# Optimization experiments

Measured on AMD Instinct MI355X. Metric: run time of the kernel, lower is better.

## Reference

```python
import jax, jax.numpy as jnp
import numpy as np

D_MODEL, D_K, D_V, N_HEADS = 1024, 64, 64, 16
B, S = 8, 1024
NEG = -1e9
LN_EPS = 1e-5


def setup_inputs() -> dict:
    key = jax.random.key(0)
    ks = jax.random.split(key, 10)
    scale = 1.0 / np.sqrt(D_MODEL)
    return {
        "Q_in": jax.random.normal(ks[0], (B, S, D_MODEL), jnp.float32),
        "K_in": jax.random.normal(ks[1], (B, S, D_MODEL), jnp.float32),
        "V_in": jax.random.normal(ks[2], (B, S, D_MODEL), jnp.float32),
        "mask": jax.random.randint(ks[3], (B, S, S), 0, 2).astype(bool),
        "W_Q": jax.random.normal(ks[4], (D_MODEL, N_HEADS * D_K), jnp.float32) * scale,
        "W_K": jax.random.normal(ks[5], (D_MODEL, N_HEADS * D_K), jnp.float32) * scale,
        "W_V": jax.random.normal(ks[6], (D_MODEL, N_HEADS * D_V), jnp.float32) * scale,
        "W_fc": jax.random.normal(ks[7], (N_HEADS * D_V, D_MODEL), jnp.float32) * scale,
        "ln_gamma": jnp.ones((D_MODEL,), jnp.float32),
        "ln_beta": jnp.zeros((D_MODEL,), jnp.float32),
    }


def reference(Q_in, K_in, V_in, mask, W_Q, W_K, W_V, W_fc, ln_gamma, ln_beta):
    b = Q_in.shape[0]
    # projections -> (B, H, S, d)
    Q = (Q_in @ W_Q).reshape(b, -1, N_HEADS, D_K).transpose(0, 2, 1, 3)
    K = (K_in @ W_K).reshape(b, -1, N_HEADS, D_K).transpose(0, 2, 1, 3)
    V = (V_in @ W_V).reshape(b, -1, N_HEADS, D_V).transpose(0, 2, 1, 3)
    # scores (B, H, Sq, Sk)
    scores = jnp.einsum("bhqd,bhkd->bhqk", Q, K) / np.sqrt(D_K)
    scores = jnp.where(mask[:, None, :, :], NEG, scores)
    attn = jax.nn.softmax(scores, axis=-1)
    context = jnp.einsum("bhqk,bhkd->bhqd", attn, V)
    context = context.transpose(0, 2, 1, 3).reshape(b, -1, N_HEADS * D_V)
    out = context @ W_fc + Q_in  # residual
    mu = jnp.mean(out, axis=-1, keepdims=True)
    var = jnp.var(out, axis=-1, keepdims=True)
    out = (out - mu) * jax.lax.rsqrt(var + LN_EPS) * ln_gamma + ln_beta
    return out, attn
```

## Files before the change

kernel.cpp:

```cpp
#include <hip/hip_runtime.h>
#include <stdint.h>

typedef unsigned short u16;
typedef float f32x4 __attribute__((ext_vector_type(4)));
typedef short s16x8 __attribute__((ext_vector_type(8)));
typedef short s16x4 __attribute__((ext_vector_type(4)));
typedef int   i32x4 __attribute__((ext_vector_type(4)));

constexpr int B  = 8;
constexpr int S  = 1024;
constexpr int DM = 1024;
constexpr int H  = 16;
constexpr int M  = B * S;
constexpr float NEGINF = -1e9f;

__device__ __forceinline__ u16 f2bf(float f) {
    union { float f; uint32_t u; } v; v.f = f;
    uint32_t u = v.u;
    uint32_t r = 0x7FFFu + ((u >> 16) & 1u);
    return (u16)((u + r) >> 16);
}
__device__ __forceinline__ float bf2f(u16 h) {
    union { uint32_t u; float f; } v; v.u = ((uint32_t)h) << 16; return v.f;
}

__device__ __forceinline__ void gload16(const u16* g, u16* l) {
    __builtin_amdgcn_global_load_lds(
        (const __attribute__((address_space(1))) unsigned int*)g,
        (__attribute__((address_space(3))) unsigned int*)l, 16, 0, 0);
}

__global__ void cvt_all(const float* __restrict__ q, const float* __restrict__ k,
                        const float* __restrict__ v,
                        u16* __restrict__ xq, u16* __restrict__ xk, u16* __restrict__ xv) {
    const float* in; u16* out;
    if (blockIdx.y == 0)      { in = q; out = xq; }
    else if (blockIdx.y == 1) { in = k; out = xk; }
    else                      { in = v; out = xv; }
    int i = (blockIdx.x * 256 + threadIdx.x) * 4;
    float4 val = *(const float4*)(in + i);
    ushort4 o;
    o.x = f2bf(val.x); o.y = f2bf(val.y); o.z = f2bf(val.z); o.w = f2bf(val.w);
    *(ushort4*)(out + i) = o;
}

__global__ void transpose_all(const float* __restrict__ w0, const float* __restrict__ w1,
                              const float* __restrict__ w2, const float* __restrict__ w3,
                              u16* __restrict__ o0, u16* __restrict__ o1,
                              u16* __restrict__ o2, u16* __restrict__ o3) {
    const float* W; u16* Wt;
    switch (blockIdx.z) {
        case 0:  W = w0; Wt = o0; break;
        case 1:  W = w1; Wt = o1; break;
        case 2:  W = w2; Wt = o2; break;
        default: W = w3; Wt = o3; break;
    }
    __shared__ float tile[32][33];
    int n0 = blockIdx.x * 32, k0 = blockIdx.y * 32;
    int tx = threadIdx.x & 31, ty = threadIdx.x >> 5;
#pragma unroll
    for (int r = 0; r < 4; ++r)
        tile[ty + r*8][tx] = W[(size_t)(k0 + ty + r*8) * DM + n0 + tx];
    __syncthreads();
#pragma unroll
    for (int r = 0; r < 4; ++r)
        Wt[(size_t)(n0 + ty + r*8) * DM + k0 + tx] = f2bf(tile[tx][ty + r*8]);
}

template<int EPI>
__global__ __launch_bounds__(256, 2)
void gemm_bt(const u16* __restrict__ A, const u16* __restrict__ Bt,
             void* __restrict__ Cv, const float* __restrict__ resid)
{
    __shared__ u16 As[128 * 32];
    __shared__ u16 Bs[128 * 32];
    const int m0 = blockIdx.x * 128;
    const int n0 = blockIdx.y * 128;
    const int t = threadIdx.x;
    const int lane = t & 63;
    const int wid = t >> 6;
    const int wm = (wid >> 1) * 64;
    const int wn = (wid & 1) * 64;
    const int lr = lane & 15;
    const int lg = lane >> 4;

    const u16* Ag = A  + (size_t)(m0 + (t >> 2)) * 1024 + (t & 3) * 8;
    const u16* Bg = Bt + (size_t)(n0 + (t >> 2)) * 1024 + (t & 3) * 8;
    u16* Al = As + t * 8;
    u16* Bl = Bs + t * 8;

    f32x4 acc[4][4] = {};

    for (int kt = 0; kt < 32; ++kt) {
        const int ko = kt * 32;
        __syncthreads();
        gload16(Ag + ko,            Al);
        gload16(Ag + 64*1024 + ko,  Al + 64*32);
        gload16(Bg + ko,            Bl);
        gload16(Bg + 64*1024 + ko,  Bl + 64*32);
        __syncthreads();
        s16x8 af[4], bfr[4];
#pragma unroll
        for (int m = 0; m < 4; ++m)
            af[m] = *(const s16x8*)(As + (wm + m*16 + lr) * 32 + lg * 8);
#pragma unroll
        for (int n = 0; n < 4; ++n)
            bfr[n] = *(const s16x8*)(Bs + (wn + n*16 + lr) * 32 + lg * 8);
#pragma unroll
        for (int m = 0; m < 4; ++m)
#pragma unroll
            for (int n = 0; n < 4; ++n)
                acc[m][n] = __builtin_amdgcn_mfma_f32_16x16x32_bf16(af[m], bfr[n], acc[m][n], 0, 0, 0);
    }

#pragma unroll
    for (int m = 0; m < 4; ++m) {
#pragma unroll
        for (int n = 0; n < 4; ++n) {
            const int rg0 = m0 + wm + m*16 + lg*4;
            const int cg  = n0 + wn + n*16 + lr;
            if constexpr (EPI == 0) {
                u16* C = (u16*)Cv;
#pragma unroll
                for (int r = 0; r < 4; ++r)
                    C[(size_t)(rg0 + r) * 1024 + cg] = f2bf(acc[m][n][r]);
            } else if constexpr (EPI == 1) {
                u16* C = (u16*)Cv;
                const int bb = rg0 >> 10;
                const int s0 = rg0 & 1023;
                const int hh = cg >> 6;
                const int dd = cg & 63;
                ushort4 pk;
                pk.x = f2bf(acc[m][n][0]); pk.y = f2bf(acc[m][n][1]);
                pk.z = f2bf(acc[m][n][2]); pk.w = f2bf(acc[m][n][3]);
                *(ushort4*)(C + (size_t)((bb*16 + hh)*64 + dd) * 1024 + s0) = pk;
            } else {
                float* C = (float*)Cv;
#pragma unroll
                for (int r = 0; r < 4; ++r) {
                    size_t idx = (size_t)(rg0 + r) * 1024 + cg;
                    C[idx] = acc[m][n][r] + resid[idx];
                }
            }
        }
    }
}

__global__ __launch_bounds__(256, 2)
void attn_fused(const u16* __restrict__ Qp, const u16* __restrict__ Kp,
                const void* __restrict__ maskp, const u16* __restrict__ Vt,
                float* __restrict__ attn, u16* __restrict__ ctx)
{
    const int i  = blockIdx.x;
    const int qt = (i >> 3) & 63;
    const int g  = ((i >> 9) << 3) | (i & 7);
    const int h  = g & 15;
    const int b  = g >> 4;
    const int q0 = qt * 16;

    const int t = threadIdx.x;
    const int lane = t & 63;
    const int w = t >> 6;
    const int lr = lane & 15;
    const int lg = lane >> 4;

    constexpr int PLD = 1032;
    __shared__ u16 Plds[16][PLD];
    __shared__ float redB[4][16];

    uint32_t orv = 0;
    const uint32_t* mw = (const uint32_t*)maskp;
#pragma unroll
    for (int ii = 0; ii < 64; ++ii) orv |= mw[ii];
    const bool mask_bytes = (orv > 1u);

    const u16* qb = Qp + (size_t)(b*S + q0 + lr) * DM + h*64 + lg*8;
    s16x8 qf0 = *(const s16x8*)(qb);
    s16x8 qf1 = *(const s16x8*)(qb + 32);

    const size_t mrow = (size_t)b * S * S + (size_t)(q0 + lr) * S;

    i32x4 kf0s[2][4], kf1s[2][4], mis[2][4];
    int   mbs[2][4];
    s16x4 paf[16];
    float hs = 0.f;

#define QK_ISSUE(st, nb_) do {                                                      \
    _Pragma("unroll")                                                               \
    for (int j = 0; j < 4; ++j) {                                                   \
        const u16* kb_ = Kp + (size_t)(b*S + w*256 + (nb_)*64 + j*16 + lr) * DM     \
                            + h*64 + lg*8;                                          \
        asm volatile("global_load_dwordx4 %0, %2, off\n\t"                          \
                     "global_load_dwordx4 %1, %2, off offset:64"                    \
                     : "=v"(kf0s[st][j]), "=v"(kf1s[st][j]) : "v"(kb_));            \
        const size_t off_ = mrow + w*256 + (nb_)*64 + j*16 + lg*4;                  \
        if (mask_bytes) {                                                           \
            asm volatile("global_load_dword %0, %1, off"                            \
                         : "=v"(mbs[st][j]) : "v"((const uint8_t*)maskp + off_));   \
        } else {                                                                    \
            asm volatile("global_load_dwordx4 %0, %1, off"                          \
                         : "=v"(mis[st][j]) : "v"((const int*)maskp + off_));       \
        }                                                                           \
    }                                                                               \
} while (0)

#define QK_COMPUTE(st, nb_) do {                                                    \
    _Pragma("unroll")                                                               \
    for (int j = 0; j < 4; ++j) {                                                   \
        const int nk_ = (nb_)*4 + j;                                                \
        s16x8 kf0 = *(const s16x8*)&kf0s[st][j];                                    \
        s16x8 kf1 = *(const s16x8*)&kf1s[st][j];                                    \
        int m0_, m1_, m2_, m3_;                                                     \
        if (mask_bytes) {                                                           \
            int mm = mbs[st][j];                                                    \
            m0_ = mm & 255; m1_ = (mm >> 8) & 255;                                  \
            m2_ = (mm >> 16) & 255; m3_ = ((unsigned)mm) >> 24;                     \
        } else {                                                                    \
            m0_ = mis[st][j][0]; m1_ = mis[st][j][1];                               \
            m2_ = mis[st][j][2]; m3_ = mis[st][j][3];                               \
        }                                                                           \
        f32x4 cc = {};                                                              \
        cc = __builtin_amdgcn_mfma_f32_16x16x32_bf16(kf0, qf0, cc, 0, 0, 0);        \
        cc = __builtin_amdgcn_mfma_f32_16x16x32_bf16(kf1, qf1, cc, 0, 0, 0);        \
        cc[0] = __expf(m0_ ? NEGINF : cc[0] * 0.125f);                              \
        cc[1] = __expf(m1_ ? NEGINF : cc[1] * 0.125f);                              \
        cc[2] = __expf(m2_ ? NEGINF : cc[2] * 0.125f);                              \
        cc[3] = __expf(m3_ ? NEGINF : cc[3] * 0.125f);                              \
        hs += cc[0] + cc[1] + cc[2] + cc[3];                                        \
        s16x4 pa;                                                                   \
        pa[0] = (short)f2bf(cc[0]); pa[1] = (short)f2bf(cc[1]);                     \
        pa[2] = (short)f2bf(cc[2]); pa[3] = (short)f2bf(cc[3]);                     \
        paf[nk_] = pa;                                                              \
        *(s16x4*)&Plds[lr][w*256 + nk_*16 + lg*4] = pa;                             \
    }                                                                               \
} while (0)

    QK_ISSUE(0, 0);
    QK_ISSUE(1, 1);
    asm volatile("s_waitcnt vmcnt(12)");
    __builtin_amdgcn_sched_barrier(0);
    QK_COMPUTE(0, 0);
    QK_ISSUE(0, 2);
    asm volatile("s_waitcnt vmcnt(12)");
    __builtin_amdgcn_sched_barrier(0);
    QK_COMPUTE(1, 1);
    QK_ISSUE(1, 3);
    asm volatile("s_waitcnt vmcnt(12)");
    __builtin_amdgcn_sched_barrier(0);
    QK_COMPUTE(0, 2);
    asm volatile("s_waitcnt vmcnt(0)");
    __builtin_amdgcn_sched_barrier(0);
    QK_COMPUTE(1, 3);
#undef QK_ISSUE
#undef QK_COMPUTE

    hs += __shfl_xor(hs, 16, 64);
    hs += __shfl_xor(hs, 32, 64);
    if (lane < 16) redB[w][lr] = hs;
    __syncthreads();

    const float tot = redB[0][lr] + redB[1][lr] + redB[2][lr] + redB[3][lr];
    const float inv  = tot > 0.f ? 1.0f / tot : 0.f;
    const float fill = tot > 0.f ? 0.f : (1.0f / 1024.0f);
    float invr[4];
#pragma unroll
    for (int r = 0; r < 4; ++r) {
        const int row = lg*4 + r;
        const float tr = redB[0][row] + redB[1][row] + redB[2][row] + redB[3][row];
        invr[r] = tr > 0.f ? 1.0f / tr : 0.f;
    }

    float* arow = attn + (size_t)(b*H + h) * S * S + (size_t)(q0 + lr) * S + w*256 + lg*4;
#pragma unroll
    for (int nk = 0; nk < 16; ++nk) {
        float4 st;
        st.x = fmaf(bf2f((u16)paf[nk][0]), inv, fill);
        st.y = fmaf(bf2f((u16)paf[nk][1]), inv, fill);
        st.z = fmaf(bf2f((u16)paf[nk][2]), inv, fill);
        st.w = fmaf(bf2f((u16)paf[nk][3]), inv, fill);
        *(float4*)(arow + nk*16) = st;
    }

    const u16* vrow = Vt + ((size_t)g*64 + w*16 + lr) * S;
    i32x4 vfs[2][8];
    f32x4 pacc = {};

#define PV_ISSUE(st, kb_) do {                                                      \
    _Pragma("unroll")                                                               \
    for (int j = 0; j < 8; ++j) {                                                   \
        asm volatile("global_load_dwordx4 %0, %1, off"                              \
                     : "=v"(vfs[st][j]) : "v"(vrow + (kb_)*256 + j*32 + lg*8));     \
    }                                                                               \
} while (0)

#define PV_COMPUTE(st, kb_) do {                                                    \
    _Pragma("unroll")                                                               \
    for (int j = 0; j < 8; ++j) {                                                   \
        s16x8 af = *(const s16x8*)&Plds[lr][((kb_)*8 + j)*32 + lg*8];               \
        s16x8 vf = *(const s16x8*)&vfs[st][j];                                      \
        pacc = __builtin_amdgcn_mfma_f32_16x16x32_bf16(af, vf, pacc, 0, 0, 0);      \
    }                                                                               \
} while (0)

    PV_ISSUE(0, 0);
    PV_ISSUE(1, 1);
    asm volatile("s_waitcnt vmcnt(8)");
    __builtin_amdgcn_sched_barrier(0);
    PV_COMPUTE(0, 0);
    PV_ISSUE(0, 2);
    asm volatile("s_waitcnt vmcnt(8)");
    __builtin_amdgcn_sched_barrier(0);
    PV_COMPUTE(1, 1);
    PV_ISSUE(1, 3);
    asm volatile("s_waitcnt vmcnt(8)");
    __builtin_amdgcn_sched_barrier(0);
    PV_COMPUTE(0, 2);
    asm volatile("s_waitcnt vmcnt(0)");
    __builtin_amdgcn_sched_barrier(0);
    PV_COMPUTE(1, 3);
#undef PV_ISSUE
#undef PV_COMPUTE

#pragma unroll
    for (int r = 0; r < 4; ++r)
        ctx[(size_t)(b*S + q0 + lg*4 + r) * DM + h*64 + w*16 + lr] = f2bf(pacc[r] * invr[r]);
}

__global__ __launch_bounds__(256)
void layernorm(const float* __restrict__ x, const float* __restrict__ gamma,
               const float* __restrict__ beta, float* __restrict__ out)
{
    const int row = blockIdx.x;
    const int t = threadIdx.x;
    const float* xr = x + (size_t)row * DM;
    float4 v = *(const float4*)(xr + t*4);
    float s  = v.x + v.y + v.z + v.w;
    float s2 = v.x*v.x + v.y*v.y + v.z*v.z + v.w*v.w;
#pragma unroll
    for (int d = 1; d < 64; d <<= 1) {
        s  += __shfl_xor(s,  d, 64);
        s2 += __shfl_xor(s2, d, 64);
    }
    __shared__ float ls[4], ls2[4];
    if ((t & 63) == 0) { ls[t >> 6] = s; ls2[t >> 6] = s2; }
    __syncthreads();
    s  = ls[0] + ls[1] + ls[2] + ls[3];
    s2 = ls2[0] + ls2[1] + ls2[2] + ls2[3];
    const float mu  = s * (1.0f / DM);
    const float var = s2 * (1.0f / DM) - mu * mu;
    const float rs  = rsqrtf(var + 1e-5f);
    float4 g  = *(const float4*)(gamma + t*4);
    float4 bb = *(const float4*)(beta  + t*4);
    float4 o;
    o.x = (v.x - mu) * rs * g.x + bb.x;
    o.y = (v.y - mu) * rs * g.y + bb.y;
    o.z = (v.z - mu) * rs * g.z + bb.z;
    o.w = (v.w - mu) * rs * g.w + bb.w;
    *(float4*)(out + (size_t)row * DM + t*4) = o;
}

extern "C" void kernel_launch(void* const* d_in, const int* in_sizes, int n_in,
                              void* d_out, int out_size, void* d_ws, size_t ws_size,
                              hipStream_t stream) {
    const float* Qin  = (const float*)d_in[0];
    const float* Kin  = (const float*)d_in[1];
    const float* Vin  = (const float*)d_in[2];
    const void*  mask = d_in[3];
    const float* Wq   = (const float*)d_in[4];
    const float* Wk   = (const float*)d_in[5];
    const float* Wv   = (const float*)d_in[6];
    const float* Wfc  = (const float*)d_in[7];
    const float* gam  = (const float*)d_in[8];
    const float* bet  = (const float*)d_in[9];

    float* out  = (float*)d_out;
    float* attn = (float*)d_out + (size_t)M * DM;

    char* ws = (char*)d_ws;
    constexpr size_t SZ_X = (size_t)M * DM * 2;
    constexpr size_t SZ_W = (size_t)DM * DM * 2;
    u16* Xq  = (u16*)(ws);
    u16* Xk  = (u16*)(ws + SZ_X);
    u16* Xv  = (u16*)(ws + 2*SZ_X);
    u16* WqT = (u16*)(ws + 3*SZ_X);
    u16* WkT = (u16*)(ws + 3*SZ_X + SZ_W);
    u16* WvT = (u16*)(ws + 3*SZ_X + 2*SZ_W);
    u16* WfT = (u16*)(ws + 3*SZ_X + 3*SZ_W);
    u16* Qp  = (u16*)(ws + 3*SZ_X + 4*SZ_W);
    u16* Kp  = (u16*)(ws + 4*SZ_X + 4*SZ_W);
    u16* Vt  = (u16*)(ws + 5*SZ_X + 4*SZ_W);
    float* preLN = (float*)(ws);
    u16*   Ctx   = (u16*)(ws + 2*SZ_X);

    dim3 blk(256);
    cvt_all<<<dim3(M * DM / 1024, 3), blk, 0, stream>>>(Qin, Kin, Vin, Xq, Xk, Xv);
    transpose_all<<<dim3(32, 32, 4), blk, 0, stream>>>(Wq, Wk, Wv, Wfc, WqT, WkT, WvT, WfT);

    gemm_bt<0><<<dim3(64, 8), blk, 0, stream>>>(Xq, WqT, Qp, nullptr);
    gemm_bt<0><<<dim3(64, 8), blk, 0, stream>>>(Xk, WkT, Kp, nullptr);
    gemm_bt<1><<<dim3(64, 8), blk, 0, stream>>>(Xv, WvT, Vt, nullptr);

    attn_fused<<<dim3(8192), blk, 0, stream>>>(Qp, Kp, mask, Vt, attn, Ctx);

    gemm_bt<2><<<dim3(64, 8), blk, 0, stream>>>(Ctx, WfT, preLN, Qin);
    layernorm<<<dim3(M), blk, 0, stream>>>(preLN, gam, bet, out);
}
```

Baseline: 548.0 us.

## Split fused attention into score kernel and separate tiled P·V GEMM

Breaks the fused attention kernel into two. The first computes and stores the normalized attention probabilities. The second is a 128x64-tiled GEMM that re-reads the fp32 attention matrix from global memory, converts it to bf16, and multiplies it by V using double-buffered LDS staging. The aim is to drop the large LDS P buffer, improve occupancy, and get V reuse across 128 query rows instead of 16. The cost is re-reading the full 512MB fp32 attention matrix, which adds a large amount of memory traffic.

```diff
diff --git a/kernel.cpp b/kernel.cpp
--- a/kernel.cpp
+++ b/kernel.cpp
@@ -147,9 +147,8 @@
 }
 
 __global__ __launch_bounds__(256, 2)
-void attn_fused(const u16* __restrict__ Qp, const u16* __restrict__ Kp,
-                const void* __restrict__ maskp, const u16* __restrict__ Vt,
-                float* __restrict__ attn, u16* __restrict__ ctx)
+void attn_scores(const u16* __restrict__ Qp, const u16* __restrict__ Kp,
+                 const void* __restrict__ maskp, float* __restrict__ attn)
 {
     const int i  = blockIdx.x;
     const int qt = (i >> 3) & 63;
@@ -164,8 +163,6 @@
     const int lr = lane & 15;
     const int lg = lane >> 4;
 
-    constexpr int PLD = 1032;
-    __shared__ u16 Plds[16][PLD];
     __shared__ float redB[4][16];
 
     uint32_t orv = 0;
@@ -231,7 +228,6 @@
         pa[0] = (short)f2bf(cc[0]); pa[1] = (short)f2bf(cc[1]);                     \
         pa[2] = (short)f2bf(cc[2]); pa[3] = (short)f2bf(cc[3]);                     \
         paf[nk_] = pa;                                                              \
-        *(s16x4*)&Plds[lr][w*256 + nk_*16 + lg*4] = pa;                             \
     }                                                                               \
 } while (0)
 
@@ -258,17 +254,9 @@
     hs += __shfl_xor(hs, 32, 64);
     if (lane < 16) redB[w][lr] = hs;
     __syncthreads();
-
     const float tot = redB[0][lr] + redB[1][lr] + redB[2][lr] + redB[3][lr];
     const float inv  = tot > 0.f ? 1.0f / tot : 0.f;
     const float fill = tot > 0.f ? 0.f : (1.0f / 1024.0f);
-    float invr[4];
-#pragma unroll
-    for (int r = 0; r < 4; ++r) {
-        const int row = lg*4 + r;
-        const float tr = redB[0][row] + redB[1][row] + redB[2][row] + redB[3][row];
-        invr[r] = tr > 0.f ? 1.0f / tr : 0.f;
-    }
 
     float* arow = attn + (size_t)(b*H + h) * S * S + (size_t)(q0 + lr) * S + w*256 + lg*4;
 #pragma unroll
@@ -280,50 +268,98 @@
         st.w = fmaf(bf2f((u16)paf[nk][3]), inv, fill);
         *(float4*)(arow + nk*16) = st;
     }
-
-    const u16* vrow = Vt + ((size_t)g*64 + w*16 + lr) * S;
-    i32x4 vfs[2][8];
-    f32x4 pacc = {};
-
-#define PV_ISSUE(st, kb_) do {                                                      \
+}
+
+__global__ __launch_bounds__(256, 2)
+void attn_pv_gemm(const float* __restrict__ attn, const u16* __restrict__ Vt,
+                  u16* __restrict__ ctx)
+{
+    __shared__ float Abuf[2][128 * 64];
+    __shared__ u16   Vbuf[2][64 * 64];
+    const int i  = blockIdx.x;
+    const int qt = (i >> 3) & 7;
+    const int g  = ((i >> 6) << 3) | (i & 7);
+    const int h  = g & 15;
+    const int b  = g >> 4;
+    const int q0 = qt * 128;
+
+    const int t = threadIdx.x;
+    const int lane = t & 63;
+    const int w = t >> 6;
+    const int lr = lane & 15;
+    const int lg = lane >> 4;
+
+    const float* abase = attn + (size_t)(b*H + h) * S * S + (size_t)q0 * S;
+    const u16*   vbase = Vt + (size_t)g * 64 * S;
+
+#define PSTAGE(bi, kk) do {                                                         \
+    const int k0_ = (kk) * 64;                                                      \
     _Pragma("unroll")                                                               \
     for (int j = 0; j < 8; ++j) {                                                   \
-        asm volatile("global_load_dwordx4 %0, %1, off"                              \
-                     : "=v"(vfs[st][j]) : "v"(vrow + (kb_)*256 + j*32 + lg*8));     \
+        const int s_ = j*256 + t;                         \
+        const int r_ = s_ >> 4;                                    \
+        const int p_ = s_ & 15;                           \
+        const int l_ = p_ ^ ((r_ & 7) << 1);      \
+        gload16((const u16*)(abase + (size_t)r_ * S + k0_ + l_*4),                  \
+                (u16*)&Abuf[bi][s_ * 4]);                                           \
+    }                                                                               \
+    _Pragma("unroll")                                                               \
+    for (int j = 0; j < 2; ++j) {                                                   \
+        const int s_ = j*256 + t;                                      \
+        const int r_ = s_ >> 3;                                          \
+        const int p_ = s_ & 7;                                                      \
+        const int l_ = p_ ^ (r_ & 7);                                               \
+        gload16(vbase + (size_t)r_ * S + k0_ + l_*8, &Vbuf[bi][s_ * 8]);            \
     }                                                                               \
 } while (0)
 
-#define PV_COMPUTE(st, kb_) do {                                                    \
-    _Pragma("unroll")                                                               \
-    for (int j = 0; j < 8; ++j) {                                                   \
-        s16x8 af = *(const s16x8*)&Plds[lr][((kb_)*8 + j)*32 + lg*8];               \
-        s16x8 vf = *(const s16x8*)&vfs[st][j];                                      \
-        pacc = __builtin_amdgcn_mfma_f32_16x16x32_bf16(af, vf, pacc, 0, 0, 0);      \
-    }                                                                               \
-} while (0)
-
-    PV_ISSUE(0, 0);
-    PV_ISSUE(1, 1);
-    asm volatile("s_waitcnt vmcnt(8)");
-    __builtin_amdgcn_sched_barrier(0);
-    PV_COMPUTE(0, 0);
-    PV_ISSUE(0, 2);
-    asm volatile("s_waitcnt vmcnt(8)");
-    __builtin_amdgcn_sched_barrier(0);
-    PV_COMPUTE(1, 1);
-    PV_ISSUE(1, 3);
-    asm volatile("s_waitcnt vmcnt(8)");
-    __builtin_amdgcn_sched_barrier(0);
-    PV_COMPUTE(0, 2);
-    asm volatile("s_waitcnt vmcnt(0)");
-    __builtin_amdgcn_sched_barrier(0);
-    PV_COMPUTE(1, 3);
-#undef PV_ISSUE
-#undef PV_COMPUTE
-
-#pragma unroll
-    for (int r = 0; r < 4; ++r)
-        ctx[(size_t)(b*S + q0 + lg*4 + r) * DM + h*64 + w*16 + lr] = f2bf(pacc[r] * invr[r]);
+    f32x4 acc[2][4] = {};
+
+    PSTAGE(0, 0);
+    __syncthreads();
+
+    for (int k = 0; k < 16; ++k) {
+        const int cur = k & 1;
+        if (k < 15) PSTAGE(cur ^ 1, k + 1);
+#pragma unroll
+        for (int ks = 0; ks < 2; ++ks) {
+            s16x8 af[2];
+#pragma unroll
+            for (int fq = 0; fq < 2; ++fq) {
+                const int row = w*32 + fq*16 + lr;
+                const int ch  = (ks*4 + lg) ^ (lr & 7);
+                const float* ap = &Abuf[cur][row*64 + ch*8];
+                float4 a0 = *(const float4*)(ap);
+                float4 a1 = *(const float4*)(ap + 4);
+                s16x8 v;
+                v[0] = (short)f2bf(a0.x); v[1] = (short)f2bf(a0.y);
+                v[2] = (short)f2bf(a0.z); v[3] = (short)f2bf(a0.w);
+                v[4] = (short)f2bf(a1.x); v[5] = (short)f2bf(a1.y);
+                v[6] = (short)f2bf(a1.z); v[7] = (short)f2bf(a1.w);
+                af[fq] = v;
+            }
+#pragma unroll
+            for (int nd = 0; nd < 4; ++nd) {
+                const int row = nd*16 + lr;
+                const int sl  = (ks*4 + lg) ^ (lr & 7);
+                s16x8 vf = *(const s16x8*)&Vbuf[cur][row*64 + sl*8];
+#pragma unroll
+                for (int fq = 0; fq < 2; ++fq)
+                    acc[fq][nd] = __builtin_amdgcn_mfma_f32_16x16x32_bf16(af[fq], vf, acc[fq][nd], 0, 0, 0);
+            }
+        }
+        __syncthreads();
+    }
+#undef PSTAGE
+
+#pragma unroll
+    for (int fq = 0; fq < 2; ++fq)
+#pragma unroll
+        for (int nd = 0; nd < 4; ++nd)
+#pragma unroll
+            for (int r = 0; r < 4; ++r)
+                ctx[(size_t)(b*S + q0 + w*32 + fq*16 + lg*4 + r) * DM + h*64 + nd*16 + lr]
+                    = f2bf(acc[fq][nd][r]);
 }
 
 __global__ __launch_bounds__(256)
@@ -400,7 +436,8 @@
     gemm_bt<0><<<dim3(64, 8), blk, 0, stream>>>(Xk, WkT, Kp, nullptr);
     gemm_bt<1><<<dim3(64, 8), blk, 0, stream>>>(Xv, WvT, Vt, nullptr);
 
-    attn_fused<<<dim3(8192), blk, 0, stream>>>(Qp, Kp, mask, Vt, attn, Ctx);
+    attn_scores<<<dim3(8192), blk, 0, stream>>>(Qp, Kp, mask, attn);
+    attn_pv_gemm<<<dim3(1024), blk, 0, stream>>>(attn, Vt, Ctx);
 
     gemm_bt<2><<<dim3(64, 8), blk, 0, stream>>>(Ctx, WfT, preLN, Qin);
     layernorm<<<dim3(M), blk, 0, stream>>>(preLN, gam, bet, out);
```

New measurement: 589.9 us. +7.6%, slower.
